# Kernel optimization log

Measured on AMD Instinct MI355X. Metric: run time of the kernel, lower is better.

## Reference

```python
import jax, jax.numpy as jnp
import numpy as np

N = 50000
E = 1600000
F_IN = 256
HEADS = 4
HID = 32
C = 16
NEG_SLOPE = 0.2


def _add_self_loops(edge_index, n):
    loop = jnp.arange(n, dtype=edge_index.dtype)
    return jnp.concatenate([edge_index, jnp.stack([loop, loop])], axis=1)


def gat_conv(x, edge_index, W, att_src, att_dst, bias, heads, n):
    # PyG GATConv (concat=True, add_self_loops=True, inference: no dropout)
    ei = _add_self_loops(edge_index, n)
    src, dst = ei[0], ei[1]
    d = W.shape[1] // heads
    xw = (x @ W).reshape(n, heads, d)                      # [N,H,D]
    a_src = jnp.sum(xw * att_src, axis=-1)                 # [N,H]
    a_dst = jnp.sum(xw * att_dst, axis=-1)                 # [N,H]
    e = jax.nn.leaky_relu(a_src[src] + a_dst[dst], NEG_SLOPE)  # [E',H]
    # segment softmax over destination neighborhoods
    m = jax.ops.segment_max(e, dst, num_segments=n)        # [N,H]
    ex = jnp.exp(e - m[dst])
    denom = jax.ops.segment_sum(ex, dst, num_segments=n)   # [N,H]
    alpha = ex / denom[dst]                                # [E',H]
    msg = xw[src] * alpha[:, :, None]                      # [E',H,D]
    out = jax.ops.segment_sum(msg, dst, num_segments=n)    # [N,H,D]
    return out.reshape(n, heads * d) + bias


def setup_inputs() -> dict:
    key = jax.random.key(0)
    ks = jax.random.split(key, 10)
    g = lambda k, shape, fan: jax.random.normal(k, shape, jnp.float32) * (1.0 / np.sqrt(fan))
    x = jax.random.normal(ks[0], (N, F_IN), jnp.float32)
    edge_index = jax.random.randint(ks[1], (2, E), 0, N, dtype=jnp.int64)
    return {
        "x": x,
        "edge_index": edge_index,
        "W1": g(ks[2], (F_IN, HEADS * HID), F_IN),
        "att_src1": g(ks[3], (HEADS, HID), HID),
        "att_dst1": g(ks[4], (HEADS, HID), HID),
        "b1": jnp.zeros((HEADS * HID,), jnp.float32),
        "W2": g(ks[5], (HEADS * HID, C), HEADS * HID),
        "att_src2": g(ks[6], (1, C), C),
        "att_dst2": g(ks[7], (1, C), C),
        "b2": jnp.zeros((C,), jnp.float32),
    }


def reference(x, edge_index, W1, att_src1, att_dst1, b1, W2, att_src2, att_dst2, b2):
    h = gat_conv(x, edge_index, W1, att_src1, att_dst1, b1, HEADS, N)
    h = jax.nn.relu(h)
    # dropout: identity at inference (training=False)
    out = gat_conv(h, edge_index, W2, att_src2, att_dst2, b2, 1, N)
    return jax.nn.log_softmax(out, axis=1)
```

## Files before the change

kernel.cpp:

```cpp
#include <hip/hip_runtime.h>
#include <hip/hip_bf16.h>

typedef __hip_bfloat16 bf16;
typedef long long i64;
typedef unsigned long long u64;
typedef __attribute__((ext_vector_type(8))) short short8;
typedef __attribute__((ext_vector_type(4))) float floatx4;

#define NN    50000
#define EE    1600000
#define E2    1650000
#define FIN   256
#define HD    128
#define NH    4
#define NC    16
#define SLOPE 0.2f
#define K     128
#define DPB   391
#define CAPB  16384
#define CAP   15360
#define CH2   2048

#define XA_W  264
#define WB_W  40
#define XW_W  72

#define OF_FLAGS 0
#define OF_BCUR  16
#define OF_BBASE 144
#define OF_RP    280
#define OF_BIN   50282
#define OF_CSR   4244586
#define OF_XW1   5894588
#define OF_AS1   9094588
#define OF_AD1   9294588
#define OF_HW2   9494588
#define OF_AS2   10294588
#define OF_AD2   10344588

__device__ __forceinline__ float b2f(bf16 v) { return __bfloat162float(v); }
__device__ __forceinline__ float us2f(unsigned short u) {
    return __uint_as_float(((unsigned)u) << 16);
}
__device__ __forceinline__ unsigned short f2us(float f) {
    unsigned u = __float_as_uint(f);
    return (unsigned short)((u + 0x7fffu + ((u >> 16) & 1u)) >> 16);
}
__device__ __forceinline__ float lrelu(float v) { return v > 0.f ? v : SLOPE * v; }

template <bool F32>
__device__ __forceinline__ float ldin(const void* p, int i) {
    if (F32) return ((const float*)p)[i];
    return b2f(((const bf16*)p)[i]);
}
template <bool F32>
__device__ __forceinline__ float4 ldin4(const void* p, int i) {
    if (F32) return *(const float4*)((const float*)p + i);
    ushort4 u = *(const ushort4*)((const unsigned short*)p + i);
    float4 r;
    r.x = us2f(u.x); r.y = us2f(u.y); r.z = us2f(u.z); r.w = us2f(u.w);
    return r;
}

__device__ __forceinline__ void edge_sd(const void* ei, int f64, int e, int& s, int& d) {
    if (e >= EE) { s = e - EE; d = s; return; }
    if (f64) {
        s = (int)((const i64*)ei)[e];
        d = (int)((const i64*)ei)[EE + e];
    } else {
        s = ((const int*)ei)[e];
        d = ((const int*)ei)[EE + e];
    }
    s = min(max(s, 0), NN - 1);
    d = min(max(d, 0), NN - 1);
}

__global__ void detect(const void* x, const void* ei, int* flags) {
    __shared__ int cnt[2];
    if (threadIdx.x == 0) { cnt[0] = 0; cnt[1] = 0; }
    __syncthreads();
    const unsigned short* xb = (const unsigned short*)x;
    int c0 = 0;
    for (int i = threadIdx.x; i < 4096; i += 256) {
        float v = __uint_as_float(((unsigned)xb[2 * i]) << 16);
        if (!(fabsf(v) < 1e6f)) c0++;
    }
    const i64* e64 = (const i64*)ei;
    int c1 = 0;
    for (int i = threadIdx.x; i < 1024; i += 256) {
        i64 v = e64[i];
        if (v >= 0 && v < NN) c1++;
    }
    atomicAdd(&cnt[0], c0);
    atomicAdd(&cnt[1], c1);
    __syncthreads();
    if (threadIdx.x == 0) {
        flags[0] = (cnt[0] > 400) ? 1 : 0;
        flags[1] = (cnt[1] >= 1000) ? 1 : 0;
    }
}

__global__ void initBcur(int* __restrict__ bcur) {
    int t = threadIdx.x;
    if (t < K) bcur[t] = t * CAPB;
}

__global__ __launch_bounds__(256) void binScatter(const void* __restrict__ ei,
                                                  const int* __restrict__ flags,
                                                  int* __restrict__ bcur,
                                                  u64* __restrict__ bin) {
    __shared__ int h[K], res[K];
    int t = threadIdx.x;
    int start = blockIdx.x * CH2;
    int endc = min(start + CH2, E2);
    if (t < K) h[t] = 0;
    __syncthreads();
    int f64 = flags[1];
    int myb[8], myr[8];
    u64 myp[8];
    int nb_ = 0;
    for (int e = start + t; e < endc; e += 256) {
        int s, d; edge_sd(ei, f64, e, s, d);
        int b = d / DPB;
        myb[nb_] = b;
        myp[nb_] = (((u64)(unsigned)d) << 32) | (unsigned)s;
        myr[nb_] = atomicAdd(&h[b], 1);
        nb_++;
    }
    __syncthreads();
    if (t < K) res[t] = h[t] ? atomicAdd(&bcur[t], h[t]) : 0;
    __syncthreads();
    for (int i = 0; i < nb_; i++) {
        int b = myb[i];
        int pos = res[b] + myr[i];
        pos = min(pos, (b + 1) * CAPB - 1);
        bin[pos] = myp[i];
    }
}

__global__ void bucketScan(const int* __restrict__ bcur, int* __restrict__ bbase) {
    __shared__ int sh[K];
    int t = threadIdx.x;
    int v = min(bcur[t] - t * CAPB, CAPB);
    sh[t] = v;
    __syncthreads();
    for (int off = 1; off < K; off <<= 1) {
        int u = (t >= off) ? sh[t - off] : 0;
        __syncthreads();
        sh[t] += u;
        __syncthreads();
    }
    bbase[t] = sh[t] - v;
    if (t == K - 1) bbase[K] = sh[K - 1];
}

__global__ __launch_bounds__(256) void csrB(const u64* __restrict__ bin,
                                            const int* __restrict__ bbase,
                                            int* __restrict__ rp, int* __restrict__ csr) {
    __shared__ int cnt[512];
    __shared__ int cur[DPB];
    __shared__ int buf[CAP];
    int b = blockIdx.x, t = threadIdx.x;
    int d0 = b * DPB;
    int nd = min(DPB, NN - d0);
    int src0 = b * CAPB;
    int base = bbase[b], size = bbase[b + 1] - base;
    cnt[t] = 0; cnt[t + 256] = 0;
    __syncthreads();
    for (int i = t; i < size; i += 256) {
        int d = (int)(bin[src0 + i] >> 32);
        atomicAdd(&cnt[d - d0], 1);
    }
    __syncthreads();
    int a0 = cnt[2 * t], a1 = cnt[2 * t + 1];
    int ps = a0 + a1;
    buf[t] = ps;
    __syncthreads();
    for (int off = 1; off < 256; off <<= 1) {
        int u = (t >= off) ? buf[t - off] : 0;
        __syncthreads();
        buf[t] += u;
        __syncthreads();
    }
    int ex = buf[t] - ps;
    __syncthreads();
    cnt[2 * t] = ex;
    cnt[2 * t + 1] = ex + a0;
    __syncthreads();
    for (int i = t; i < nd; i += 256) {
        rp[d0 + i] = base + cnt[i];
        cur[i] = cnt[i];
    }
    if (b == K - 1 && t == 0) rp[NN] = bbase[K];
    __syncthreads();
    if (size <= CAP) {
        for (int i = t; i < size; i += 256) {
            u64 p = bin[src0 + i];
            int pos = atomicAdd(&cur[(int)(p >> 32) - d0], 1);
            buf[pos] = (int)(unsigned)p;
        }
        __syncthreads();
        for (int i = t; i < size; i += 256) csr[base + i] = buf[i];
    } else {
        for (int i = t; i < size; i += 256) {
            u64 p = bin[src0 + i];
            int pos = base + atomicAdd(&cur[(int)(p >> 32) - d0], 1);
            csr[pos] = (int)(unsigned)p;
        }
    }
}

template <bool F32>
__global__ __launch_bounds__(256) void gemm1(
    const void* __restrict__ x, const void* __restrict__ W1,
    const void* __restrict__ as1, const void* __restrict__ ad1,
    const int* __restrict__ flags, unsigned short* __restrict__ xwb,
    float* __restrict__ asrc, float* __restrict__ adst) {
    if ((flags[0] != 0) != F32) return;
    __shared__ unsigned short xa[64 * XA_W];
    __shared__ unsigned short wb[8 * 64 * WB_W];
    int t = threadIdx.x;
    int mb = blockIdx.x >> 1, nb = blockIdx.x & 1;
    int m0 = mb * 64, n0 = nb * 64;
#pragma unroll
    for (int i = 0; i < 16; i++) {
        int slot = i * 256 + t;
        int mi = slot >> 6, k4 = (slot & 63) * 4;
        float4 v = make_float4(0.f, 0.f, 0.f, 0.f);
        if (m0 + mi < NN) v = ldin4<F32>(x, (m0 + mi) * FIN + k4);
        ushort4 o;
        o.x = f2us(v.x); o.y = f2us(v.y); o.z = f2us(v.z); o.w = f2us(v.w);
        *(ushort4*)&xa[mi * XA_W + k4] = o;
    }
#pragma unroll
    for (int i = 0; i < 16; i++) {
        int k = i * 16 + (t >> 4);
        int ni = (t & 15) * 4;
        float4 v = ldin4<F32>(W1, k * HD + n0 + ni);
        int ks = k >> 5, kk = k & 31;
        wb[(ks * 64 + ni + 0) * WB_W + kk] = f2us(v.x);
        wb[(ks * 64 + ni + 1) * WB_W + kk] = f2us(v.y);
        wb[(ks * 64 + ni + 2) * WB_W + kk] = f2us(v.z);
        wb[(ks * 64 + ni + 3) * WB_W + kk] = f2us(v.w);
    }
    __syncthreads();
    int w = t >> 6, lane = t & 63;
    int col = lane & 15, q = lane >> 4;
    floatx4 dacc[4];
#pragma unroll
    for (int mt = 0; mt < 4; mt++) { dacc[mt].x = 0.f; dacc[mt].y = 0.f; dacc[mt].z = 0.f; dacc[mt].w = 0.f; }
#pragma unroll
    for (int ks = 0; ks < 8; ks++) {
        short8 bf = *(const short8*)&wb[(ks * 64 + w * 16 + col) * WB_W + q * 8];
#pragma unroll
        for (int mt = 0; mt < 4; mt++) {
            short8 af = *(const short8*)&xa[(mt * 16 + col) * XA_W + ks * 32 + q * 8];
            dacc[mt] = __builtin_amdgcn_mfma_f32_16x16x32_bf16(af, bf, dacc[mt], 0, 0, 0);
        }
    }
    __syncthreads();
    unsigned short* xw = xa;
#pragma unroll
    for (int mt = 0; mt < 4; mt++) {
#pragma unroll
        for (int r = 0; r < 4; r++) {
            int nloc = mt * 16 + q * 4 + r;
            xw[nloc * XW_W + w * 16 + col] = f2us(dacc[mt][r]);
        }
    }
    __syncthreads();
#pragma unroll
    for (int i = 0; i < 2; i++) {
        int chunk = i * 256 + t;
        int node = chunk >> 3, oct = chunk & 7;
        if (m0 + node < NN) {
            uint4 v = *(const uint4*)&xw[node * XW_W + oct * 8];
            *(uint4*)&xwb[(m0 + node) * HD + n0 + oct * 8] = v;
        }
    }
    {
        int node = t >> 2, hh = (t >> 1) & 1, half = t & 1;
        if (m0 + node < NN) {
            float s = 0.f, dd = 0.f;
            int cb = hh * 32 + half * 16;
#pragma unroll
            for (int c = 0; c < 16; c++) {
                float xv = us2f(xw[node * XW_W + cb + c]);
                s  += xv * ldin<F32>(as1, n0 + cb + c);
                dd += xv * ldin<F32>(ad1, n0 + cb + c);
            }
            s  += __shfl_xor(s, 1);
            dd += __shfl_xor(dd, 1);
            if (half == 0) {
                int head = nb * 2 + hh;
                asrc[(m0 + node) * NH + head] = s;
                adst[(m0 + node) * NH + head] = dd;
            }
        }
    }
}

template <bool F32>
__global__ __launch_bounds__(128) void node1(
    const int* __restrict__ rp, const int* __restrict__ cs,
    const float* __restrict__ asrc, const float* __restrict__ adst,
    const unsigned short* __restrict__ xwb, const void* __restrict__ b1,
    const void* __restrict__ W2, const void* __restrict__ as2, const void* __restrict__ ad2,
    const int* __restrict__ flags, float* __restrict__ hw2,
    float* __restrict__ asrc2, float* __restrict__ adst2) {
    if ((flags[0] != 0) != F32) return;
    int d = blockIdx.x, t = threadIdx.x;
    int beg = rp[d], end = rp[d + 1];
    __shared__ float sw[32][4];
    __shared__ int   ss[32];
    __shared__ float red[2][HD];
    __shared__ float wred[2][16];
    __shared__ float hs[HD];
    __shared__ float l2[32];
    int hw_ = t & 3;
    float adw = adst[d * NH + hw_];
    int cg = t & 15, eo = t >> 4, head = cg >> 2;
    float acc[8];
#pragma unroll
    for (int j = 0; j < 8; j++) acc[j] = 0.f;
    float wsum = 0.f;
    for (int chb = beg; chb < end; chb += 32) {
        __syncthreads();
        int ec = chb + (t >> 2);
        float w = 0.f;
        int s = 0;
        if (ec < end) {
            s = cs[ec];
            w = __expf(fminf(lrelu(asrc[s * NH + hw_] + adw), 80.f));
        }
        sw[t >> 2][hw_] = w;
        if (hw_ == 0) ss[t >> 2] = s;
        __syncthreads();
        int m = min(32, end - chb);
        for (int e = eo; e < m; e += 8) {
            float we = sw[e][head];
            int s2 = ss[e];
            uint4 u = *(const uint4*)&xwb[s2 * HD + cg * 8];
            acc[0] += we * __uint_as_float(u.x << 16);
            acc[1] += we * __uint_as_float(u.x & 0xffff0000u);
            acc[2] += we * __uint_as_float(u.y << 16);
            acc[3] += we * __uint_as_float(u.y & 0xffff0000u);
            acc[4] += we * __uint_as_float(u.z << 16);
            acc[5] += we * __uint_as_float(u.z & 0xffff0000u);
            acc[6] += we * __uint_as_float(u.w << 16);
            acc[7] += we * __uint_as_float(u.w & 0xffff0000u);
            wsum += we;
        }
    }
#pragma unroll
    for (int j = 0; j < 8; j++) {
        acc[j] += __shfl_xor(acc[j], 16);
        acc[j] += __shfl_xor(acc[j], 32);
    }
    wsum += __shfl_xor(wsum, 16);
    wsum += __shfl_xor(wsum, 32);
    int wid = t >> 6, lane = t & 63;
    if (lane < 16) {
        wred[wid][lane] = wsum;
#pragma unroll
        for (int j = 0; j < 8; j++) red[wid][lane * 8 + j] = acc[j];
    }
    __syncthreads();
    float tot = red[0][t] + red[1][t];
    float wt  = wred[0][t >> 3] + wred[1][t >> 3];
    hs[t] = fmaxf(tot / wt + ldin<F32>(b1, t), 0.f);
    __syncthreads();
    int j = t & 15, g = t >> 4;
    float p = 0.f;
#pragma unroll
    for (int k = 0; k < 16; k++) p += hs[g * 16 + k] * ldin<F32>(W2, (g * 16 + k) * NC + j);
    p += __shfl_xor(p, 16, 64);
    p += __shfl_xor(p, 32, 64);
    if ((t & 63) < 16) l2[(t >> 6) * 16 + j] = p;
    __syncthreads();
    if (t < 16) {
        float hw = l2[t] + l2[16 + t];
        hw2[d * NC + t] = hw;
        float a2s = hw * ldin<F32>(as2, t);
        float a2d = hw * ldin<F32>(ad2, t);
#pragma unroll
        for (int off = 8; off; off >>= 1) {
            a2s += __shfl_xor(a2s, off, 16);
            a2d += __shfl_xor(a2d, off, 16);
        }
        if (t == 0) { asrc2[d] = a2s; adst2[d] = a2d; }
    }
}

template <bool F32>
__global__ __launch_bounds__(64) void node2(
    const int* __restrict__ rp, const int* __restrict__ cs,
    const float* __restrict__ asrc2, const float* __restrict__ adst2,
    const float* __restrict__ hw2, const void* __restrict__ b2,
    const int* __restrict__ flags, void* __restrict__ out) {
    if ((flags[0] != 0) != F32) return;
    int d = blockIdx.x, t = threadIdx.x;
    int beg = rp[d], end = rp[d + 1];
    float ad = adst2[d];
    __shared__ float sw2[64];
    __shared__ int   ss2[64];
    int q = t & 3, eo = t >> 2;
    float4 acc = make_float4(0.f, 0.f, 0.f, 0.f);
    float wsum = 0.f;
    for (int chb = beg; chb < end; chb += 64) {
        __syncthreads();
        int ec = chb + t;
        float w = 0.f;
        int s = 0;
        if (ec < end) {
            s = cs[ec];
            w = __expf(fminf(lrelu(asrc2[s] + ad), 80.f));
        }
        sw2[t] = w;
        ss2[t] = s;
        __syncthreads();
        int m = min(64, end - chb);
        for (int e = eo; e < m; e += 16) {
            float we = sw2[e];
            float4 v = *(const float4*)&hw2[ss2[e] * NC + q * 4];
            acc.x += we * v.x; acc.y += we * v.y;
            acc.z += we * v.z; acc.w += we * v.w;
            wsum += we;
        }
    }
#pragma unroll
    for (int off = 4; off < 64; off <<= 1) {
        acc.x += __shfl_xor(acc.x, off);
        acc.y += __shfl_xor(acc.y, off);
        acc.z += __shfl_xor(acc.z, off);
        acc.w += __shfl_xor(acc.w, off);
        wsum  += __shfl_xor(wsum, off);
    }
    float rw = 1.f / wsum;
    float v0 = acc.x * rw + ldin<F32>(b2, q * 4 + 0);
    float v1 = acc.y * rw + ldin<F32>(b2, q * 4 + 1);
    float v2 = acc.z * rw + ldin<F32>(b2, q * 4 + 2);
    float v3 = acc.w * rw + ldin<F32>(b2, q * 4 + 3);
    float mx = fmaxf(fmaxf(v0, v1), fmaxf(v2, v3));
    mx = fmaxf(mx, __shfl_xor(mx, 1));
    mx = fmaxf(mx, __shfl_xor(mx, 2));
    float es = __expf(v0 - mx) + __expf(v1 - mx) + __expf(v2 - mx) + __expf(v3 - mx);
    es += __shfl_xor(es, 1);
    es += __shfl_xor(es, 2);
    float lse = mx + __logf(es);
    if (t < 4) {
        if (F32) {
            *(float4*)&((float*)out)[d * NC + q * 4] =
                make_float4(v0 - lse, v1 - lse, v2 - lse, v3 - lse);
        } else {
            bf16* o = (bf16*)out + d * NC + q * 4;
            o[0] = __float2bfloat16(v0 - lse); o[1] = __float2bfloat16(v1 - lse);
            o[2] = __float2bfloat16(v2 - lse); o[3] = __float2bfloat16(v3 - lse);
        }
    }
}

extern "C" void kernel_launch(void* const* d_in, const int* in_sizes, int n_in,
                              void* d_out, int out_size, void* d_ws, size_t ws_size,
                              hipStream_t stream) {
    const void* x   = d_in[0];
    const void* ei  = d_in[1];
    const void* W1  = d_in[2];
    const void* as1 = d_in[3];
    const void* ad1 = d_in[4];
    const void* b1  = d_in[5];
    const void* W2  = d_in[6];
    const void* as2 = d_in[7];
    const void* ad2 = d_in[8];
    const void* b2v = d_in[9];

    float* ws = (float*)d_ws;
    int* flags = (int*)(ws + OF_FLAGS);
    int* bcur  = (int*)(ws + OF_BCUR);
    int* bbase = (int*)(ws + OF_BBASE);
    int* rp    = (int*)(ws + OF_RP);
    u64* bin   = (u64*)(ws + OF_BIN);
    int* csr   = (int*)(ws + OF_CSR);
    unsigned short* xwb = (unsigned short*)(ws + OF_XW1);
    float* asrc1 = ws + OF_AS1;
    float* adst1 = ws + OF_AD1;
    float* hw2   = ws + OF_HW2;
    float* asrc2 = ws + OF_AS2;
    float* adst2 = ws + OF_AD2;

    detect<<<1, 256, 0, stream>>>(x, ei, flags);
    initBcur<<<1, 128, 0, stream>>>(bcur);
    binScatter<<<(E2 + CH2 - 1) / CH2, 256, 0, stream>>>(ei, flags, bcur, bin);
    bucketScan<<<1, K, 0, stream>>>(bcur, bbase);
    csrB<<<K, 256, 0, stream>>>(bin, bbase, rp, csr);

    const int GB = ((NN + 63) / 64) * 2;
    gemm1<true><<<GB, 256, 0, stream>>>(x, W1, as1, ad1, flags, xwb, asrc1, adst1);
    node1<true><<<NN, 128, 0, stream>>>(rp, csr, asrc1, adst1, xwb, b1, W2, as2, ad2,
                                        flags, hw2, asrc2, adst2);
    node2<true><<<NN, 64, 0, stream>>>(rp, csr, asrc2, adst2, hw2, b2v, flags, d_out);
}
```

Baseline: 321.4 us.

## Quantize layer-1 features to int8 with per-node scales, vectorize edge binning

The first-layer projected features are now stored as int8 with a per-node, per-half scale instead of bf16. This halves the bytes each edge gather reads in the aggregation kernel, and the scale is folded into the attention weight, which is why the weight sum is now tracked separately. The GEMM shared layout is reorganized to be fragment-major, and edge binning now loads 8 edges per thread with vector int4 loads. The initBcur kernel is merged into detect to save a launch. The int8 quantization adds numerical error that could exceed tolerance.

```diff
diff --git a/kernel.cpp b/kernel.cpp
--- a/kernel.cpp
+++ b/kernel.cpp
@@ -21,9 +21,8 @@
 #define CAP   15360
 #define CH2   2048
 
-#define XA_W  264
-#define WB_W  40
-#define XW_W  72
+#define FR_W  36
+#define FW_W  68
 
 #define OF_FLAGS 0
 #define OF_BCUR  16
@@ -31,7 +30,8 @@
 #define OF_RP    280
 #define OF_BIN   50282
 #define OF_CSR   4244586
-#define OF_XW1   5894588
+#define OF_XQ    5894588
+#define OF_SC    7494588
 #define OF_AS1   9094588
 #define OF_AD1   9294588
 #define OF_HW2   9494588
@@ -47,6 +47,9 @@
     return (unsigned short)((u + 0x7fffu + ((u >> 16) & 1u)) >> 16);
 }
 __device__ __forceinline__ float lrelu(float v) { return v > 0.f ? v : SLOPE * v; }
+__device__ __forceinline__ float sb2f(unsigned u, int sh) {
+    return (float)((int)(u << (24 - sh)) >> 24);
+}
 
 template <bool F32>
 __device__ __forceinline__ float ldin(const void* p, int i) {
@@ -75,34 +78,31 @@
     d = min(max(d, 0), NN - 1);
 }
 
-__global__ void detect(const void* x, const void* ei, int* flags) {
+__global__ void detect(const void* x, const void* ei, int* flags, int* bcur) {
     __shared__ int cnt[2];
-    if (threadIdx.x == 0) { cnt[0] = 0; cnt[1] = 0; }
+    int t = threadIdx.x;
+    if (t < K) bcur[t] = t * CAPB;
+    if (t == 0) { cnt[0] = 0; cnt[1] = 0; }
     __syncthreads();
     const unsigned short* xb = (const unsigned short*)x;
     int c0 = 0;
-    for (int i = threadIdx.x; i < 4096; i += 256) {
+    for (int i = t; i < 4096; i += 256) {
         float v = __uint_as_float(((unsigned)xb[2 * i]) << 16);
         if (!(fabsf(v) < 1e6f)) c0++;
     }
     const i64* e64 = (const i64*)ei;
     int c1 = 0;
-    for (int i = threadIdx.x; i < 1024; i += 256) {
+    for (int i = t; i < 1024; i += 256) {
         i64 v = e64[i];
         if (v >= 0 && v < NN) c1++;
     }
     atomicAdd(&cnt[0], c0);
     atomicAdd(&cnt[1], c1);
     __syncthreads();
-    if (threadIdx.x == 0) {
+    if (t == 0) {
         flags[0] = (cnt[0] > 400) ? 1 : 0;
         flags[1] = (cnt[1] >= 1000) ? 1 : 0;
     }
-}
-
-__global__ void initBcur(int* __restrict__ bcur) {
-    int t = threadIdx.x;
-    if (t < K) bcur[t] = t * CAPB;
 }
 
 __global__ __launch_bounds__(256) void binScatter(const void* __restrict__ ei,
@@ -111,30 +111,48 @@
                                                   u64* __restrict__ bin) {
     __shared__ int h[K], res[K];
     int t = threadIdx.x;
-    int start = blockIdx.x * CH2;
-    int endc = min(start + CH2, E2);
+    int base = blockIdx.x * CH2 + t * 8;
     if (t < K) h[t] = 0;
     __syncthreads();
     int f64 = flags[1];
-    int myb[8], myr[8];
-    u64 myp[8];
-    int nb_ = 0;
-    for (int e = start + t; e < endc; e += 256) {
-        int s, d; edge_sd(ei, f64, e, s, d);
-        int b = d / DPB;
-        myb[nb_] = b;
-        myp[nb_] = (((u64)(unsigned)d) << 32) | (unsigned)s;
-        myr[nb_] = atomicAdd(&h[b], 1);
-        nb_++;
-    }
+    int sv[8], dv[8], rk[8];
+    int n_ = 0;
+    if (!f64 && base + 8 <= EE) {
+        const int* es = (const int*)ei;
+        int4 a = *(const int4*)&es[base];
+        int4 b = *(const int4*)&es[base + 4];
+        int4 c = *(const int4*)&es[EE + base];
+        int4 g = *(const int4*)&es[EE + base + 4];
+        sv[0] = a.x; sv[1] = a.y; sv[2] = a.z; sv[3] = a.w;
+        sv[4] = b.x; sv[5] = b.y; sv[6] = b.z; sv[7] = b.w;
+        dv[0] = c.x; dv[1] = c.y; dv[2] = c.z; dv[3] = c.w;
+        dv[4] = g.x; dv[5] = g.y; dv[6] = g.z; dv[7] = g.w;
+#pragma unroll
+        for (int i = 0; i < 8; i++) {
+            sv[i] = min(max(sv[i], 0), NN - 1);
+            dv[i] = min(max(dv[i], 0), NN - 1);
+        }
+        n_ = 8;
+    } else {
+        for (int i = 0; i < 8; i++) {
+            int e = base + i;
+            if (e < E2) {
+                int s, d; edge_sd(ei, f64, e, s, d);
+                sv[n_] = s; dv[n_] = d; n_++;
+            }
+        }
+    }
+#pragma unroll 8
+    for (int i = 0; i < n_; i++) rk[i] = atomicAdd(&h[dv[i] / DPB], 1);
     __syncthreads();
     if (t < K) res[t] = h[t] ? atomicAdd(&bcur[t], h[t]) : 0;
     __syncthreads();
-    for (int i = 0; i < nb_; i++) {
-        int b = myb[i];
-        int pos = res[b] + myr[i];
+#pragma unroll 8
+    for (int i = 0; i < n_; i++) {
+        int b = dv[i] / DPB;
+        int pos = res[b] + rk[i];
         pos = min(pos, (b + 1) * CAPB - 1);
-        bin[pos] = myp[i];
+        bin[pos] = (((u64)(unsigned)dv[i]) << 32) | (unsigned)sv[i];
     }
 }
 
@@ -214,11 +232,12 @@
 __global__ __launch_bounds__(256) void gemm1(
     const void* __restrict__ x, const void* __restrict__ W1,
     const void* __restrict__ as1, const void* __restrict__ ad1,
-    const int* __restrict__ flags, unsigned short* __restrict__ xwb,
+    const int* __restrict__ flags, signed char* __restrict__ xq, float* __restrict__ sc2,
     float* __restrict__ asrc, float* __restrict__ adst) {
     if ((flags[0] != 0) != F32) return;
-    __shared__ unsigned short xa[64 * XA_W];
-    __shared__ unsigned short wb[8 * 64 * WB_W];
+    __shared__ unsigned short af[8 * 64 * FR_W];
+    __shared__ unsigned short wb[8 * 64 * FR_W];
+    __shared__ float scl[64];
     int t = threadIdx.x;
     int mb = blockIdx.x >> 1, nb = blockIdx.x & 1;
     int m0 = mb * 64, n0 = nb * 64;
@@ -230,7 +249,7 @@
         if (m0 + mi < NN) v = ldin4<F32>(x, (m0 + mi) * FIN + k4);
         ushort4 o;
         o.x = f2us(v.x); o.y = f2us(v.y); o.z = f2us(v.z); o.w = f2us(v.w);
-        *(ushort4*)&xa[mi * XA_W + k4] = o;
+        *(ushort4*)&af[((k4 >> 5) * 64 + mi) * FR_W + (k4 & 31)] = o;
     }
 #pragma unroll
     for (int i = 0; i < 16; i++) {
@@ -238,10 +257,10 @@
         int ni = (t & 15) * 4;
         float4 v = ldin4<F32>(W1, k * HD + n0 + ni);
         int ks = k >> 5, kk = k & 31;
-        wb[(ks * 64 + ni + 0) * WB_W + kk] = f2us(v.x);
-        wb[(ks * 64 + ni + 1) * WB_W + kk] = f2us(v.y);
-        wb[(ks * 64 + ni + 2) * WB_W + kk] = f2us(v.z);
-        wb[(ks * 64 + ni + 3) * WB_W + kk] = f2us(v.w);
+        wb[(ks * 64 + ni + 0) * FR_W + kk] = f2us(v.x);
+        wb[(ks * 64 + ni + 1) * FR_W + kk] = f2us(v.y);
+        wb[(ks * 64 + ni + 2) * FR_W + kk] = f2us(v.z);
+        wb[(ks * 64 + ni + 3) * FR_W + kk] = f2us(v.w);
     }
     __syncthreads();
     int w = t >> 6, lane = t & 63;
@@ -251,31 +270,55 @@
     for (int mt = 0; mt < 4; mt++) { dacc[mt].x = 0.f; dacc[mt].y = 0.f; dacc[mt].z = 0.f; dacc[mt].w = 0.f; }
 #pragma unroll
     for (int ks = 0; ks < 8; ks++) {
-        short8 bf = *(const short8*)&wb[(ks * 64 + w * 16 + col) * WB_W + q * 8];
+        short8 bf = *(const short8*)&wb[(ks * 64 + w * 16 + col) * FR_W + q * 8];
 #pragma unroll
         for (int mt = 0; mt < 4; mt++) {
-            short8 af = *(const short8*)&xa[(mt * 16 + col) * XA_W + ks * 32 + q * 8];
-            dacc[mt] = __builtin_amdgcn_mfma_f32_16x16x32_bf16(af, bf, dacc[mt], 0, 0, 0);
-        }
-    }
-    __syncthreads();
-    unsigned short* xw = xa;
+            short8 afr = *(const short8*)&af[(ks * 64 + mt * 16 + col) * FR_W + q * 8];
+            dacc[mt] = __builtin_amdgcn_mfma_f32_16x16x32_bf16(afr, bf, dacc[mt], 0, 0, 0);
+        }
+    }
+    __syncthreads();
+    float* fw = (float*)af;
 #pragma unroll
     for (int mt = 0; mt < 4; mt++) {
 #pragma unroll
         for (int r = 0; r < 4; r++) {
             int nloc = mt * 16 + q * 4 + r;
-            xw[nloc * XW_W + w * 16 + col] = f2us(dacc[mt][r]);
-        }
-    }
-    __syncthreads();
-#pragma unroll
-    for (int i = 0; i < 2; i++) {
-        int chunk = i * 256 + t;
-        int node = chunk >> 3, oct = chunk & 7;
+            fw[nloc * FW_W + w * 16 + col] = dacc[mt][r];
+        }
+    }
+    __syncthreads();
+    {
+        int node = t >> 2, part = t & 3;
+        float amax = 0.f;
+#pragma unroll
+        for (int c = 0; c < 16; c++) amax = fmaxf(amax, fabsf(fw[node * FW_W + part * 16 + c]));
+        amax = fmaxf(amax, __shfl_xor(amax, 1));
+        amax = fmaxf(amax, __shfl_xor(amax, 2));
+        if (part == 0) {
+            scl[node] = (amax > 0.f) ? 127.f / amax : 0.f;
+            if (m0 + node < NN) sc2[(m0 + node) * 2 + nb] = amax * (1.f / 127.f);
+        }
+    }
+    __syncthreads();
+    {
+        int node = t >> 2, part = t & 3;
         if (m0 + node < NN) {
-            uint4 v = *(const uint4*)&xw[node * XW_W + oct * 8];
-            *(uint4*)&xwb[(m0 + node) * HD + n0 + oct * 8] = v;
+            float inv = scl[node];
+            unsigned dw[4];
+#pragma unroll
+            for (int g = 0; g < 4; g++) {
+                unsigned pk = 0;
+#pragma unroll
+                for (int j = 0; j < 4; j++) {
+                    float v = fw[node * FW_W + part * 16 + g * 4 + j];
+                    int qi = (int)rintf(v * inv);
+                    qi = min(127, max(-127, qi));
+                    pk |= ((unsigned)(qi & 255)) << (8 * j);
+                }
+                dw[g] = pk;
+            }
+            *(uint4*)&xq[(m0 + node) * HD + n0 + part * 16] = make_uint4(dw[0], dw[1], dw[2], dw[3]);
         }
     }
     {
@@ -285,7 +328,7 @@
             int cb = hh * 32 + half * 16;
 #pragma unroll
             for (int c = 0; c < 16; c++) {
-                float xv = us2f(xw[node * XW_W + cb + c]);
+                float xv = fw[node * FW_W + cb + c];
                 s  += xv * ldin<F32>(as1, n0 + cb + c);
                 dd += xv * ldin<F32>(ad1, n0 + cb + c);
             }
@@ -304,8 +347,9 @@
 __global__ __launch_bounds__(128) void node1(
     const int* __restrict__ rp, const int* __restrict__ cs,
     const float* __restrict__ asrc, const float* __restrict__ adst,
-    const unsigned short* __restrict__ xwb, const void* __restrict__ b1,
-    const void* __restrict__ W2, const void* __restrict__ as2, const void* __restrict__ ad2,
+    const signed char* __restrict__ xq, const float* __restrict__ sc2,
+    const void* __restrict__ b1, const void* __restrict__ W2,
+    const void* __restrict__ as2, const void* __restrict__ ad2,
     const int* __restrict__ flags, float* __restrict__ hw2,
     float* __restrict__ asrc2, float* __restrict__ adst2) {
     if ((flags[0] != 0) != F32) return;
@@ -314,7 +358,7 @@
     __shared__ float sw[32][4];
     __shared__ int   ss[32];
     __shared__ float red[2][HD];
-    __shared__ float wred[2][16];
+    __shared__ float wv[2][4];
     __shared__ float hs[HD];
     __shared__ float l2[32];
     int hw_ = t & 3;
@@ -323,51 +367,55 @@
     float acc[8];
 #pragma unroll
     for (int j = 0; j < 8; j++) acc[j] = 0.f;
-    float wsum = 0.f;
+    float wacc = 0.f;
+    const unsigned* xqu = (const unsigned*)xq;
     for (int chb = beg; chb < end; chb += 32) {
         __syncthreads();
         int ec = chb + (t >> 2);
-        float w = 0.f;
+        float w = 0.f, wsc = 0.f;
         int s = 0;
         if (ec < end) {
             s = cs[ec];
             w = __expf(fminf(lrelu(asrc[s * NH + hw_] + adw), 80.f));
-        }
-        sw[t >> 2][hw_] = w;
+            wsc = w * sc2[s * 2 + (hw_ >> 1)];
+        }
+        sw[t >> 2][hw_] = wsc;
         if (hw_ == 0) ss[t >> 2] = s;
+        wacc += w;
         __syncthreads();
         int m = min(32, end - chb);
         for (int e = eo; e < m; e += 8) {
             float we = sw[e][head];
             int s2 = ss[e];
-            uint4 u = *(const uint4*)&xwb[s2 * HD + cg * 8];
-            acc[0] += we * __uint_as_float(u.x << 16);
-            acc[1] += we * __uint_as_float(u.x & 0xffff0000u);
-            acc[2] += we * __uint_as_float(u.y << 16);
-            acc[3] += we * __uint_as_float(u.y & 0xffff0000u);
-            acc[4] += we * __uint_as_float(u.z << 16);
-            acc[5] += we * __uint_as_float(u.z & 0xffff0000u);
-            acc[6] += we * __uint_as_float(u.w << 16);
-            acc[7] += we * __uint_as_float(u.w & 0xffff0000u);
-            wsum += we;
-        }
-    }
+            uint2 u = *(const uint2*)&xqu[s2 * 32 + cg * 2];
+            acc[0] += we * sb2f(u.x, 0);
+            acc[1] += we * sb2f(u.x, 8);
+            acc[2] += we * sb2f(u.x, 16);
+            acc[3] += we * sb2f(u.x, 24);
+            acc[4] += we * sb2f(u.y, 0);
+            acc[5] += we * sb2f(u.y, 8);
+            acc[6] += we * sb2f(u.y, 16);
+            acc[7] += we * sb2f(u.y, 24);
+        }
+    }
+    wacc += __shfl_xor(wacc, 4);
+    wacc += __shfl_xor(wacc, 8);
+    wacc += __shfl_xor(wacc, 16);
+    wacc += __shfl_xor(wacc, 32);
+    int wid = t >> 6, lane = t & 63;
+    if (lane < 4) wv[wid][lane] = wacc;
 #pragma unroll
     for (int j = 0; j < 8; j++) {
         acc[j] += __shfl_xor(acc[j], 16);
         acc[j] += __shfl_xor(acc[j], 32);
     }
-    wsum += __shfl_xor(wsum, 16);
-    wsum += __shfl_xor(wsum, 32);
-    int wid = t >> 6, lane = t & 63;
     if (lane < 16) {
-        wred[wid][lane] = wsum;
 #pragma unroll
         for (int j = 0; j < 8; j++) red[wid][lane * 8 + j] = acc[j];
     }
     __syncthreads();
     float tot = red[0][t] + red[1][t];
-    float wt  = wred[0][t >> 3] + wred[1][t >> 3];
+    float wt  = wv[0][t >> 5] + wv[1][t >> 5];
     hs[t] = fmaxf(tot / wt + ldin<F32>(b1, t), 0.f);
     __syncthreads();
     int j = t & 15, g = t >> 4;
@@ -481,22 +529,22 @@
     int* rp    = (int*)(ws + OF_RP);
     u64* bin   = (u64*)(ws + OF_BIN);
     int* csr   = (int*)(ws + OF_CSR);
-    unsigned short* xwb = (unsigned short*)(ws + OF_XW1);
+    signed char* xq = (signed char*)(ws + OF_XQ);
+    float* sc2   = ws + OF_SC;
     float* asrc1 = ws + OF_AS1;
     float* adst1 = ws + OF_AD1;
     float* hw2   = ws + OF_HW2;
     float* asrc2 = ws + OF_AS2;
     float* adst2 = ws + OF_AD2;
 
-    detect<<<1, 256, 0, stream>>>(x, ei, flags);
-    initBcur<<<1, 128, 0, stream>>>(bcur);
+    detect<<<1, 256, 0, stream>>>(x, ei, flags, bcur);
     binScatter<<<(E2 + CH2 - 1) / CH2, 256, 0, stream>>>(ei, flags, bcur, bin);
     bucketScan<<<1, K, 0, stream>>>(bcur, bbase);
     csrB<<<K, 256, 0, stream>>>(bin, bbase, rp, csr);
 
     const int GB = ((NN + 63) / 64) * 2;
-    gemm1<true><<<GB, 256, 0, stream>>>(x, W1, as1, ad1, flags, xwb, asrc1, adst1);
-    node1<true><<<NN, 128, 0, stream>>>(rp, csr, asrc1, adst1, xwb, b1, W2, as2, ad2,
+    gemm1<true><<<GB, 256, 0, stream>>>(x, W1, as1, ad1, flags, xq, sc2, asrc1, adst1);
+    node1<true><<<NN, 128, 0, stream>>>(rp, csr, asrc1, adst1, xq, sc2, b1, W2, as2, ad2,
                                         flags, hw2, asrc2, adst2);
     node2<true><<<NN, 64, 0, stream>>>(rp, csr, asrc2, adst2, hw2, b2v, flags, d_out);
 }
```

Result: faster. 306.2 us (-4.8%).
